# Kernel tuning notes

Hardware: AMD Instinct MI355X
Metric: run time of the kernel (lower is better)

Reference implementation:

```python
import jax, jax.numpy as jnp
import numpy as np

B, V, M, L, D, OUT = 16, 16, 32, 24, 128, 193
VOCAB = {'cond': 5000, 'proc': 2000, 'drug': 600, 'lab_item': 700, 'lab_value': 200, 'inj_item': 400, 'inj_value': 200}


def setup_inputs() -> dict:
    key = jax.random.key(0)
    ks = iter(jax.random.split(key, 48))
    def emb_table(v):
        t = 0.02 * jax.random.normal(next(ks), (v, D), jnp.float32)
        return t.at[0].set(0.0)  # padding_idx = 0
    inp = {}
    inp['tok_cond'] = jax.random.randint(next(ks), (B, V, L), 0, VOCAB['cond'])
    inp['tok_proc'] = jax.random.randint(next(ks), (B, V, L), 0, VOCAB['proc'])
    inp['tok_drug'] = jax.random.randint(next(ks), (B, V, L), 0, VOCAB['drug'])
    inp['tok_lab_item'] = jax.random.randint(next(ks), (B, V, M, L), 0, VOCAB['lab_item'])
    inp['tok_lab_value'] = jax.random.randint(next(ks), (B, V, M, L), 0, VOCAB['lab_value'])
    inp['tok_inj_item'] = jax.random.randint(next(ks), (B, V, M, L), 0, VOCAB['inj_item'])
    inp['tok_inj_value'] = jax.random.randint(next(ks), (B, V, M, L), 0, VOCAB['inj_value'])
    inp['weight'] = jax.random.uniform(next(ks), (B, V, 1), jnp.float32)
    inp['age'] = jax.random.uniform(next(ks), (B, V, 1), jnp.float32)
    for n in ['cond', 'proc', 'drug', 'lab_item', 'lab_value', 'inj_item', 'inj_value']:
        inp['emb_' + n] = emb_table(VOCAB[n])
    def gru_params(nk):
        s = 0.05
        return (s * jax.random.normal(next(ks), (nk, 3 * D, D), jnp.float32),
                s * jax.random.normal(next(ks), (nk, 3 * D, D), jnp.float32),
                jnp.zeros((nk, 3 * D), jnp.float32),
                jnp.zeros((nk, 3 * D), jnp.float32))
    inp['mgru_wih'], inp['mgru_whh'], inp['mgru_bih'], inp['mgru_bhh'] = gru_params(5)
    inp['vgru_wih'], inp['vgru_whh'], inp['vgru_bih'], inp['vgru_bhh'] = gru_params(7)
    inp['info_w'] = 0.05 * jax.random.normal(next(ks), (2, D), jnp.float32)  # Linear(1, D) weights for weight/age
    inp['info_b'] = jnp.zeros((2, D), jnp.float32)
    inp['fc_w'] = 0.05 * jax.random.normal(next(ks), (7 * D, OUT), jnp.float32)
    inp['fc_b'] = jnp.zeros((OUT,), jnp.float32)
    return inp


def _gru(x, wih, whh, bih, bhh):
    # x: [N, T, Din]; torch nn.GRU semantics, gate order (r, z, n), h0 = 0
    n_, t_, _ = x.shape
    d = whh.shape[1]
    xg = jnp.einsum('ntd,gd->ntg', x, wih) + bih  # precompute input gates [N, T, 3D]
    def step(h, xg_t):
        gh = h @ whh.T + bhh
        ir, iz, inn = jnp.split(xg_t, 3, axis=-1)
        hr, hz, hn = jnp.split(gh, 3, axis=-1)
        r = jax.nn.sigmoid(ir + hr)
        z = jax.nn.sigmoid(iz + hz)
        n = jnp.tanh(inn + r * hn)
        h2 = (1.0 - z) * n + z * h
        return h2, h2
    h0 = jnp.zeros((n_, d), x.dtype)
    hT, outs = jax.lax.scan(step, h0, jnp.swapaxes(xg, 0, 1))
    return jnp.swapaxes(outs, 0, 1), hT  # output [N,T,D], hidden [N,D]

_gru_keys = jax.vmap(_gru)  # vmap over the per-feature-key leading axis


def reference(tok_cond, tok_proc, tok_drug, tok_lab_item, tok_lab_value, tok_inj_item, tok_inj_value,
              weight, age, emb_cond, emb_proc, emb_drug, emb_lab_item, emb_lab_value, emb_inj_item,
              emb_inj_value, mgru_wih, mgru_whh, mgru_bih, mgru_bhh, vgru_wih, vgru_whh, vgru_bih,
              vgru_bhh, info_w, info_b, fc_w, fc_b):
    b, v, m, _ = tok_lab_item.shape
    d = emb_cond.shape[1]
    # visit-event features: embedding + sum over code dim (dropout = identity, eval mode)
    e_cond = emb_cond[tok_cond].sum(axis=2)  # [B,V,D]
    e_proc = emb_proc[tok_proc].sum(axis=2)
    e_drug = emb_drug[tok_drug].sum(axis=2)
    # monitor-event pairs: elementwise mul of the two embeddings, sum over code dim
    lab = (emb_lab_item[tok_lab_item] * emb_lab_value[tok_lab_value]).sum(axis=3)  # [B,V,M,D]
    inj = (emb_inj_item[tok_inj_item] * emb_inj_value[tok_inj_value]).sum(axis=3)
    # repeat visit embeddings across the monitor axis (repeat(1, max_monitors, 1))
    rep = lambda e: jnp.broadcast_to(e[:, :, None, :], (b, v, m, d))
    mon_in = jnp.stack([rep(e_cond), rep(e_proc), rep(e_drug), lab, inj], axis=0)
    mon_in = mon_in.reshape(5, b * v, m, d)  # aggregate_tensors with uniform lengths
    # per-key monitor-level GRUs
    mon_out, mon_h = _gru_keys(mon_in, mgru_wih, mgru_whh, mgru_bih, mgru_bhh)
    # split_tensor + extract_and_transpose: take last monitor step per visit -> [5,B,V,D]
    last = mon_out[:, :, -1, :].reshape(5, b, v, d)
    # patient info Linear(1, D) for weight / age
    w_emb = weight * info_w[0] + info_b[0]  # [B,V,D]
    a_emb = age * info_w[1] + info_b[1]
    vis_in = jnp.concatenate([last, jnp.stack([w_emb, a_emb], axis=0)], axis=0)  # [7,B,V,D]
    # per-key visit-level GRUs
    _, vis_h = _gru_keys(vis_in, vgru_wih, vgru_whh, vgru_bih, vgru_bhh)  # [7,B,D]
    patient_emb = jnp.transpose(vis_h, (1, 0, 2)).reshape(b, 7 * d)  # concatenate_patient_embeddings
    logits = jax.nn.relu(patient_emb) @ fc_w + fc_b  # fc_patient: ReLU -> Linear(7D, output_size)
    return logits
```

## Files before the change

### kernel.cpp

```cpp
#include <hip/hip_runtime.h>
#include <stdint.h>

typedef unsigned short u16;
typedef unsigned int u32;

#define B_ 16
#define V_ 16
#define M_ 32
#define L_ 24
#define D_ 128
#define G_ 384
#define N_ 256
#define NM_ 8192
#define OUT_ 193

using bf16x8 = __attribute__((ext_vector_type(8))) __bf16;
using floatx4 = __attribute__((ext_vector_type(4))) float;
using u16x4 = __attribute__((ext_vector_type(4))) u16;

__device__ __forceinline__ float bf2f(u16 u) {
  u32 x = ((u32)u) << 16;
  return __builtin_bit_cast(float, x);
}
__device__ __forceinline__ u16 f2bf(float f) {
  u32 u = __builtin_bit_cast(u32, f);
  u = (u + 0x7FFFu + ((u >> 16) & 1u)) >> 16;
  return (u16)u;
}
__device__ __forceinline__ float sigm_(float x) {
  return __builtin_amdgcn_rcpf(1.0f + __expf(-x));
}
__device__ __forceinline__ float tanh_(float x) {
  float e = __expf(2.0f * x);
  return 1.0f - 2.0f * __builtin_amdgcn_rcpf(e + 1.0f);
}
__device__ __forceinline__ floatx4 mfma16(bf16x8 a, bf16x8 b, floatx4 c) {
  return __builtin_amdgcn_mfma_f32_16x16x32_bf16(a, b, c, 0, 0, 0);
}
__device__ __forceinline__ void stage16(const u16* gsrc, u16* ldst) {
  __builtin_amdgcn_global_load_lds(
      (const __attribute__((address_space(1))) void*)gsrc,
      (__attribute__((address_space(3))) void*)ldst, 16, 0, 0);
}

__device__ __forceinline__ void split4(floatx4 v, u16* __restrict__ hip, u16* __restrict__ lop) {
  u16x4 h, l;
#pragma unroll
  for (int k = 0; k < 4; k++) {
    u16 hb = f2bf(v[k]);
    h[k] = hb;
    l[k] = f2bf(v[k] - bf2f(hb));
  }
  *(u16x4*)hip = h;
  *(u16x4*)lop = l;
}

#define CONVB 1152
#define VEB 32
#define PEB 1024

__global__ __launch_bounds__(256) void k_stage1(
    const int* __restrict__ tc, const int* __restrict__ tp, const int* __restrict__ td,
    const int* __restrict__ tli, const int* __restrict__ tlv,
    const int* __restrict__ tii, const int* __restrict__ tiv,
    const float* __restrict__ ec, const float* __restrict__ ep, const float* __restrict__ ed,
    const float* __restrict__ eli, const float* __restrict__ elv,
    const float* __restrict__ eii, const float* __restrict__ eiv,
    const float* __restrict__ wv, const float* __restrict__ av,
    const float* __restrict__ iw, const float* __restrict__ ib,
    const float* __restrict__ mwih, const float* __restrict__ vwih,
    const float* __restrict__ mwhh, const float* __restrict__ vwhh,
    u16* __restrict__ wih_hi, u16* __restrict__ whh_hi,
    u16* __restrict__ ce_hi, u16* __restrict__ ce_lo,
    u16* __restrict__ vx_hi, u16* __restrict__ vx_lo,
    u16* __restrict__ mx_hi, u16* __restrict__ mx_lo) {
  int blk = blockIdx.x, tid = threadIdx.x;
  if (blk < CONVB) {
    const int SW = 12 * G_ * D_, S5 = 5 * G_ * D_;
    int i4 = (blk * 256 + tid) * 4;
    floatx4 v;
    u16* dst;
    if (i4 < SW) {
      v = *(const floatx4*)(i4 < S5 ? mwih + i4 : vwih + (i4 - S5));
      dst = wih_hi + i4;
    } else {
      int o = i4 - SW;
      v = *(const floatx4*)(o < S5 ? mwhh + o : vwhh + (o - S5));
      dst = whh_hi + o;
    }
    u16x4 h;
#pragma unroll
    for (int k = 0; k < 4; k++) h[k] = f2bf(v[k]);
    *(u16x4*)dst = h;
  } else if (blk < CONVB + VEB) {
    int n = (blk - CONVB) * 8 + (tid >> 5);
    int j = tid & 31;
    floatx4 a0 = {0.f, 0.f, 0.f, 0.f}, a1 = a0, a2 = a0;
#pragma unroll 4
    for (int l = 0; l < L_; l++) {
      a0 += *(const floatx4*)(ec + (size_t)tc[n * L_ + l] * D_ + j * 4);
      a1 += *(const floatx4*)(ep + (size_t)tp[n * L_ + l] * D_ + j * 4);
      a2 += *(const floatx4*)(ed + (size_t)td[n * L_ + l] * D_ + j * 4);
    }
    size_t o0 = (size_t)n * D_ + j * 4;
    split4(a0, ce_hi + o0, ce_lo + o0);
    split4(a1, ce_hi + (size_t)N_ * D_ + o0, ce_lo + (size_t)N_ * D_ + o0);
    split4(a2, ce_hi + (size_t)2 * N_ * D_ + o0, ce_lo + (size_t)2 * N_ * D_ + o0);
    float wq = wv[n], aq = av[n];
    floatx4 iw0 = *(const floatx4*)(iw + j * 4);
    floatx4 iw1 = *(const floatx4*)(iw + D_ + j * 4);
    floatx4 ib0 = *(const floatx4*)(ib + j * 4);
    floatx4 ib1 = *(const floatx4*)(ib + D_ + j * 4);
    floatx4 v1 = wq * iw0 + ib0;
    floatx4 v2 = aq * iw1 + ib1;
    split4(v1, vx_hi + (size_t)5 * N_ * D_ + o0, vx_lo + (size_t)5 * N_ * D_ + o0);
    split4(v2, vx_hi + (size_t)6 * N_ * D_ + o0, vx_lo + (size_t)6 * N_ * D_ + o0);
  } else {
    int r = (blk - CONVB - VEB) * 8 + (tid >> 5);
    int j = tid & 31;
    floatx4 al4 = {0.f, 0.f, 0.f, 0.f}, ai4 = al4;
#pragma unroll 4
    for (int l = 0; l < L_; l++) {
      al4 += *(const floatx4*)(eli + (size_t)tli[r * L_ + l] * D_ + j * 4) *
             *(const floatx4*)(elv + (size_t)tlv[r * L_ + l] * D_ + j * 4);
      ai4 += *(const floatx4*)(eii + (size_t)tii[r * L_ + l] * D_ + j * 4) *
             *(const floatx4*)(eiv + (size_t)tiv[r * L_ + l] * D_ + j * 4);
    }
    size_t o = (size_t)r * D_ + j * 4;
    split4(al4, mx_hi + o, mx_lo + o);
    split4(ai4, mx_hi + (size_t)NM_ * D_ + o, mx_lo + (size_t)NM_ * D_ + o);
  }
}

template <int MODE, int TT>
__global__ __launch_bounds__(512, 1) void k_gru8(
    int cpk,
    const u16* __restrict__ xa_hi, const u16* __restrict__ xa_lo,
    const u16* __restrict__ xb_hi, const u16* __restrict__ xb_lo,
    const u16* __restrict__ wih_all, const float* __restrict__ bih_all,
    const u16* __restrict__ whh_all, const float* __restrict__ bhh_all,
    u16* __restrict__ out_hi, u16* __restrict__ out_lo, float* __restrict__ out_f32) {
  int key = blockIdx.x / cpk;
  int chunk = blockIdx.x - key * cpk;
  int n0 = chunk * 16;
  const u16* whh = whh_all + (size_t)key * (G_ * D_);
  const u16* wih = wih_all + (size_t)key * (G_ * D_);

  __shared__ __align__(16) u16 hls[2][2][16 * 128];
  __shared__ __align__(16) u16 xls[2][2][16 * 128];

  int tid = threadIdx.x;
  int w = tid >> 6, lane = tid & 63, mq = lane & 15, q = lane >> 4;
  int dA = (w << 4) + mq;

  int sp = tid >> 8, sr = (tid >> 4) & 15, sc = tid & 15;
  u16* ldst0 = &xls[0][0][0] + (size_t)sp * (16 * 128) + (sr * 16 + sc) * 8;
  u16* ldst1 = &xls[1][0][0] + (size_t)sp * (16 * 128) + (sr * 16 + sc) * 8;
  const bool constx = (MODE == 0) && (key < 3);
  const u16* gsrc;
  {
    const u16* hi;
    const u16* lo;
    size_t grow;
    if (MODE == 0) {
      if (key < 3) { hi = xa_hi; lo = xa_lo; grow = (size_t)key * N_ + n0 + sr; }
      else         { hi = xb_hi; lo = xb_lo; grow = (size_t)(key - 3) * NM_ + (size_t)(n0 + sr) * M_; }
    } else {
      hi = xa_hi; lo = xa_lo; grow = (size_t)key * N_ + sr * 16;
    }
    gsrc = (sp ? lo : hi) + grow * D_ + ((sc ^ sr) * 8);
  }

  bf16x8 bw[3][4], wf[3][4];
#pragma unroll
  for (int g = 0; g < 3; g++)
#pragma unroll
    for (int kk = 0; kk < 4; kk++) {
      size_t ro = (size_t)(g * 128 + dA) * D_ + kk * 32 + q * 8;
      bw[g][kk] = *(const bf16x8*)(whh + ro);
      wf[g][kk] = *(const bf16x8*)(wih + ro);
    }
  floatx4 bseed[3], bxs[3];
#pragma unroll
  for (int g = 0; g < 3; g++) {
    float bh = bhh_all[key * G_ + g * 128 + dA];
    float bi = bih_all[key * G_ + g * 128 + dA];
    bseed[g] = {bh, bh, bh, bh};
    bxs[g] = {bi, bi, bi, bi};
  }

  stage16(gsrc, ldst0);
  __syncthreads();

  floatx4 accx[3];
  if (constx) {
    const u16* xp0 = &xls[0][0][0];
    const u16* xp1 = &xls[0][1][0];
    bf16x8 xh[4], xl[4];
#pragma unroll
    for (int kk = 0; kk < 4; kk++) {
      int off = mq * 128 + (((kk * 4 + q) ^ mq) * 8);
      xh[kk] = *(const bf16x8*)(xp0 + off);
      xl[kk] = *(const bf16x8*)(xp1 + off);
    }
#pragma unroll
    for (int g = 0; g < 3; g++) {
      floatx4 a = mfma16(xh[0], wf[g][0], bxs[g]);
      a = mfma16(xl[0], wf[g][0], a);
      a = mfma16(xh[1], wf[g][1], a);
      a = mfma16(xl[1], wf[g][1], a);
      a = mfma16(xh[2], wf[g][2], a);
      a = mfma16(xl[2], wf[g][2], a);
      a = mfma16(xh[3], wf[g][3], a);
      accx[g] = mfma16(xl[3], wf[g][3], a);
    }
  }

  float h_old[4];
#pragma unroll
  for (int k = 0; k < 4; k++) h_old[k] = 0.f;

#pragma unroll 2
  for (int t = 0; t < TT; ++t) {
    int slot = t & 1;
    if (!constx && (t + 1 < TT))
      stage16(gsrc + (size_t)(t + 1) * D_, slot ? ldst0 : ldst1);
    if (!constx) {
      const u16* xp0 = &xls[slot][0][0];
      const u16* xp1 = &xls[slot][1][0];
      bf16x8 xh[4], xl[4];
#pragma unroll
      for (int kk = 0; kk < 4; kk++) {
        int off = mq * 128 + (((kk * 4 + q) ^ mq) * 8);
        xh[kk] = *(const bf16x8*)(xp0 + off);
        xl[kk] = *(const bf16x8*)(xp1 + off);
      }
#pragma unroll
      for (int g = 0; g < 3; g++) {
        floatx4 a = mfma16(xh[0], wf[g][0], bxs[g]);
        a = mfma16(xl[0], wf[g][0], a);
        a = mfma16(xh[1], wf[g][1], a);
        a = mfma16(xl[1], wf[g][1], a);
        a = mfma16(xh[2], wf[g][2], a);
        a = mfma16(xl[2], wf[g][2], a);
        a = mfma16(xh[3], wf[g][3], a);
        accx[g] = mfma16(xl[3], wf[g][3], a);
      }
    }
    floatx4 acch[3];
    if (t > 0) {
      const u16* hp0 = &hls[(t - 1) & 1][0][0];
      const u16* hp1 = &hls[(t - 1) & 1][1][0];
      bf16x8 ah[4], al[4];
#pragma unroll
      for (int kk = 0; kk < 4; kk++) {
        int off = mq * 128 + (((kk * 4 + q) ^ mq) * 8);
        ah[kk] = *(const bf16x8*)(hp0 + off);
        al[kk] = *(const bf16x8*)(hp1 + off);
      }
#pragma unroll
      for (int g = 0; g < 3; g++) {
        floatx4 a = mfma16(ah[0], bw[g][0], bseed[g]);
        a = mfma16(al[0], bw[g][0], a);
        a = mfma16(ah[1], bw[g][1], a);
        a = mfma16(al[1], bw[g][1], a);
        a = mfma16(ah[2], bw[g][2], a);
        a = mfma16(al[2], bw[g][2], a);
        a = mfma16(ah[3], bw[g][3], a);
        acch[g] = mfma16(al[3], bw[g][3], a);
      }
    } else {
#pragma unroll
      for (int g = 0; g < 3; g++) acch[g] = bseed[g];
    }
    u16* wrh = &hls[slot][0][0];
    u16* wrl = &hls[slot][1][0];
#pragma unroll
    for (int i = 0; i < 4; i++) {
      int row = q * 4 + i;
      float r = sigm_(accx[0][i] + acch[0][i]);
      float z = sigm_(accx[1][i] + acch[1][i]);
      float nn = tanh_(accx[2][i] + r * acch[2][i]);
      float h2 = (1.0f - z) * nn + z * h_old[i];
      h_old[i] = h2;
      u32 ub = __builtin_bit_cast(u32, h2);
      u16 hb = (u16)(ub >> 16);
      float rem = h2 - __builtin_bit_cast(float, ub & 0xFFFF0000u);
      u16 lb = f2bf(rem);
      if (t == TT - 1) {
        if (MODE == 0) {
          size_t o = ((size_t)key * N_ + n0 + row) * D_ + dA;
          out_hi[o] = hb;
          out_lo[o] = lb;
        } else {
          out_f32[((size_t)key * 16 + row) * D_ + dA] = h2;
        }
      } else {
        int idx = row * 128 + (((dA >> 3) ^ row) * 8) + (dA & 7);
        wrh[idx] = hb;
        wrl[idx] = lb;
      }
    }
    if (t + 1 < TT) __syncthreads();
  }
}

__global__ __launch_bounds__(256) void k_fc(
    const float* __restrict__ vis_h, const float* __restrict__ fc_w,
    const float* __restrict__ fc_b, float* __restrict__ out) {
  int b = blockIdx.x;
  int cg = blockIdx.y;
  int tid = threadIdx.x;
  int j = tid & 15, s = tid >> 4;
  int c = cg * 16 + j;
  bool cv = c < OUT_;

  __shared__ float hbuf[7 * D_];
  __shared__ float red[16][16];
  for (int i = tid; i < 7 * D_; i += 256) {
    float v = vis_h[((size_t)(i >> 7) * 16 + b) * D_ + (i & 127)];
    hbuf[i] = v > 0.f ? v : 0.f;
  }
  __syncthreads();

  float acc = 0.f;
  if (cv) {
    const float* wp = fc_w + (size_t)(s * 56) * OUT_ + c;
#pragma unroll 8
    for (int k = 0; k < 56; k++) acc += hbuf[s * 56 + k] * wp[(size_t)k * OUT_];
  }
  red[s][j] = acc;
  __syncthreads();
  if (s == 0 && cv) {
    float t = 0.f;
#pragma unroll
    for (int m = 0; m < 16; m++) t += red[m][j];
    out[(size_t)b * OUT_ + c] = t + fc_b[c];
  }
}

extern "C" void kernel_launch(void* const* d_in, const int* in_sizes, int n_in,
                              void* d_out, int out_size, void* d_ws, size_t ws_size,
                              hipStream_t stream) {
  (void)in_sizes; (void)n_in; (void)out_size; (void)ws_size;
  const int* tok_cond = (const int*)d_in[0];
  const int* tok_proc = (const int*)d_in[1];
  const int* tok_drug = (const int*)d_in[2];
  const int* tok_lab_item = (const int*)d_in[3];
  const int* tok_lab_value = (const int*)d_in[4];
  const int* tok_inj_item = (const int*)d_in[5];
  const int* tok_inj_value = (const int*)d_in[6];
  const float* weight = (const float*)d_in[7];
  const float* age = (const float*)d_in[8];
  const float* emb_cond = (const float*)d_in[9];
  const float* emb_proc = (const float*)d_in[10];
  const float* emb_drug = (const float*)d_in[11];
  const float* emb_lab_item = (const float*)d_in[12];
  const float* emb_lab_value = (const float*)d_in[13];
  const float* emb_inj_item = (const float*)d_in[14];
  const float* emb_inj_value = (const float*)d_in[15];
  const float* mgru_wih = (const float*)d_in[16];
  const float* mgru_whh = (const float*)d_in[17];
  const float* mgru_bih = (const float*)d_in[18];
  const float* mgru_bhh = (const float*)d_in[19];
  const float* vgru_wih = (const float*)d_in[20];
  const float* vgru_whh = (const float*)d_in[21];
  const float* vgru_bih = (const float*)d_in[22];
  const float* vgru_bhh = (const float*)d_in[23];
  const float* info_w = (const float*)d_in[24];
  const float* info_b = (const float*)d_in[25];
  const float* fc_w = (const float*)d_in[26];
  const float* fc_b = (const float*)d_in[27];

  char* p = (char*)d_ws;
  auto take = [&](size_t bytes) { char* r = p; p += (bytes + 255) & ~(size_t)255; return r; };
  u16* mx_hi = (u16*)take((size_t)2 * NM_ * D_ * 2);
  u16* mx_lo = (u16*)take((size_t)2 * NM_ * D_ * 2);
  u16* ce_hi = (u16*)take((size_t)3 * N_ * D_ * 2);
  u16* ce_lo = (u16*)take((size_t)3 * N_ * D_ * 2);
  u16* vx_hi = (u16*)take((size_t)7 * N_ * D_ * 2);
  u16* vx_lo = (u16*)take((size_t)7 * N_ * D_ * 2);
  float* vis_h = (float*)take((size_t)7 * 16 * D_ * 4);
  u16* wih_hi = (u16*)take((size_t)12 * G_ * D_ * 2);
  u16* whh_hi = (u16*)take((size_t)12 * G_ * D_ * 2);

  k_stage1<<<CONVB + VEB + PEB, 256, 0, stream>>>(
      tok_cond, tok_proc, tok_drug, tok_lab_item, tok_lab_value, tok_inj_item, tok_inj_value,
      emb_cond, emb_proc, emb_drug, emb_lab_item, emb_lab_value, emb_inj_item, emb_inj_value,
      weight, age, info_w, info_b, mgru_wih, vgru_wih, mgru_whh, vgru_whh,
      wih_hi, whh_hi, ce_hi, ce_lo, vx_hi, vx_lo, mx_hi, mx_lo);
  k_gru8<0, 32><<<80, 512, 0, stream>>>(16, ce_hi, ce_lo, mx_hi, mx_lo,
                                        wih_hi, mgru_bih, whh_hi, mgru_bhh,
                                        vx_hi, vx_lo, nullptr);
  k_gru8<1, 16><<<7, 512, 0, stream>>>(1, vx_hi, vx_lo, nullptr, nullptr,
                                       wih_hi + (size_t)5 * G_ * D_, vgru_bih,
                                       whh_hi + (size_t)5 * G_ * D_, vgru_bhh,
                                       nullptr, nullptr, vis_h);
  k_fc<<<dim3(B_, 13), 256, 0, stream>>>(vis_h, fc_w, fc_b, (float*)d_out);
}
```

Before: 224.5 us.

## Fuse monitor and visit GRU kernels with per-key atomic flag dependencies

Merges the monitor-level GRU launch (80 blocks) and the visit-level GRU launch (7 blocks) into one 87-block kernel. Visit blocks for keys 5-6 (weight/age) start at once, and visit blocks for keys 0-4 spin on a per-key atomic counter until all 16 monitor chunks for that key have written their outputs. This removes one kernel launch and the global barrier between the two stages, and lets unrelated keys overlap. The cost is a memset per call and spin-wait blocks that occupy CUs, which relies on all 87 blocks being co-resident to avoid deadlock.

```diff
diff --git a/kernel.cpp b/kernel.cpp
--- a/kernel.cpp
+++ b/kernel.cpp
@@ -133,29 +133,24 @@
 }
 
 template <int MODE, int TT>
-__global__ __launch_bounds__(512, 1) void k_gru8(
-    int cpk,
+__device__ __forceinline__ void gru_body(
+    int key, int n0,
     const u16* __restrict__ xa_hi, const u16* __restrict__ xa_lo,
     const u16* __restrict__ xb_hi, const u16* __restrict__ xb_lo,
     const u16* __restrict__ wih_all, const float* __restrict__ bih_all,
     const u16* __restrict__ whh_all, const float* __restrict__ bhh_all,
-    u16* __restrict__ out_hi, u16* __restrict__ out_lo, float* __restrict__ out_f32) {
-  int key = blockIdx.x / cpk;
-  int chunk = blockIdx.x - key * cpk;
-  int n0 = chunk * 16;
+    u16* __restrict__ out_hi, u16* __restrict__ out_lo, float* __restrict__ out_f32,
+    u16* hls_, u16* xls_) {
   const u16* whh = whh_all + (size_t)key * (G_ * D_);
   const u16* wih = wih_all + (size_t)key * (G_ * D_);
-
-  __shared__ __align__(16) u16 hls[2][2][16 * 128];
-  __shared__ __align__(16) u16 xls[2][2][16 * 128];
 
   int tid = threadIdx.x;
   int w = tid >> 6, lane = tid & 63, mq = lane & 15, q = lane >> 4;
   int dA = (w << 4) + mq;
 
   int sp = tid >> 8, sr = (tid >> 4) & 15, sc = tid & 15;
-  u16* ldst0 = &xls[0][0][0] + (size_t)sp * (16 * 128) + (sr * 16 + sc) * 8;
-  u16* ldst1 = &xls[1][0][0] + (size_t)sp * (16 * 128) + (sr * 16 + sc) * 8;
+  u16* ldst0 = xls_ + (size_t)sp * (16 * 128) + (sr * 16 + sc) * 8;
+  u16* ldst1 = xls_ + (size_t)(2 + sp) * (16 * 128) + (sr * 16 + sc) * 8;
   const bool constx = (MODE == 0) && (key < 3);
   const u16* gsrc;
   {
@@ -194,8 +189,8 @@
 
   floatx4 accx[3];
   if (constx) {
-    const u16* xp0 = &xls[0][0][0];
-    const u16* xp1 = &xls[0][1][0];
+    const u16* xp0 = xls_;
+    const u16* xp1 = xls_ + (16 * 128);
     bf16x8 xh[4], xl[4];
 #pragma unroll
     for (int kk = 0; kk < 4; kk++) {
@@ -226,8 +221,8 @@
     if (!constx && (t + 1 < TT))
       stage16(gsrc + (size_t)(t + 1) * D_, slot ? ldst0 : ldst1);
     if (!constx) {
-      const u16* xp0 = &xls[slot][0][0];
-      const u16* xp1 = &xls[slot][1][0];
+      const u16* xp0 = xls_ + (size_t)(slot * 2) * (16 * 128);
+      const u16* xp1 = xls_ + (size_t)(slot * 2 + 1) * (16 * 128);
       bf16x8 xh[4], xl[4];
 #pragma unroll
       for (int kk = 0; kk < 4; kk++) {
@@ -249,8 +244,8 @@
     }
     floatx4 acch[3];
     if (t > 0) {
-      const u16* hp0 = &hls[(t - 1) & 1][0][0];
-      const u16* hp1 = &hls[(t - 1) & 1][1][0];
+      const u16* hp0 = hls_ + (size_t)(((t - 1) & 1) * 2) * (16 * 128);
+      const u16* hp1 = hls_ + (size_t)(((t - 1) & 1) * 2 + 1) * (16 * 128);
       bf16x8 ah[4], al[4];
 #pragma unroll
       for (int kk = 0; kk < 4; kk++) {
@@ -273,8 +268,8 @@
 #pragma unroll
       for (int g = 0; g < 3; g++) acch[g] = bseed[g];
     }
-    u16* wrh = &hls[slot][0][0];
-    u16* wrl = &hls[slot][1][0];
+    u16* wrh = hls_ + (size_t)(slot * 2) * (16 * 128);
+    u16* wrl = hls_ + (size_t)(slot * 2 + 1) * (16 * 128);
 #pragma unroll
     for (int i = 0; i < 4; i++) {
       int row = q * 4 + i;
@@ -302,6 +297,44 @@
       }
     }
     if (t + 1 < TT) __syncthreads();
+  }
+}
+
+__global__ __launch_bounds__(512, 1) void k_mega(
+    const u16* __restrict__ ce_hi, const u16* __restrict__ ce_lo,
+    const u16* __restrict__ mx_hi, const u16* __restrict__ mx_lo,
+    u16* vx_hi, u16* vx_lo,
+    const u16* __restrict__ wih_m, const float* __restrict__ bih_m,
+    const u16* __restrict__ whh_m, const float* __restrict__ bhh_m,
+    const u16* __restrict__ wih_v, const float* __restrict__ bih_v,
+    const u16* __restrict__ whh_v, const float* __restrict__ bhh_v,
+    float* __restrict__ vis_h, u32* flags) {
+  __shared__ __align__(16) u16 hls[2][2][16 * 128];
+  __shared__ __align__(16) u16 xls[2][2][16 * 128];
+  int blk = blockIdx.x;
+  if (blk < 80) {
+    int key = blk >> 4, chunk = blk & 15;
+    gru_body<0, 32>(key, chunk * 16, ce_hi, ce_lo, mx_hi, mx_lo,
+                    wih_m, bih_m, whh_m, bhh_m,
+                    vx_hi, vx_lo, nullptr, &hls[0][0][0], &xls[0][0][0]);
+    __syncthreads();
+    if (threadIdx.x == 0) {
+      __threadfence();
+      __hip_atomic_fetch_add(&flags[key], 1u, __ATOMIC_RELEASE, __HIP_MEMORY_SCOPE_AGENT);
+    }
+  } else {
+    int key = blk - 80;
+    if (key < 5) {
+      if (threadIdx.x == 0) {
+        while (__hip_atomic_load(&flags[key], __ATOMIC_ACQUIRE, __HIP_MEMORY_SCOPE_AGENT) < 16u)
+          __builtin_amdgcn_s_sleep(8);
+      }
+      __syncthreads();
+      __threadfence();
+    }
+    gru_body<1, 16>(key, 0, vx_hi, vx_lo, nullptr, nullptr,
+                    wih_v, bih_v, whh_v, bhh_v,
+                    nullptr, nullptr, vis_h, &hls[0][0][0], &xls[0][0][0]);
   }
 }
 
@@ -383,18 +416,19 @@
   float* vis_h = (float*)take((size_t)7 * 16 * D_ * 4);
   u16* wih_hi = (u16*)take((size_t)12 * G_ * D_ * 2);
   u16* whh_hi = (u16*)take((size_t)12 * G_ * D_ * 2);
+  u32* flags = (u32*)take(256);
+
+  hipMemsetAsync(flags, 0, 64, stream);
 
   k_stage1<<<CONVB + VEB + PEB, 256, 0, stream>>>(
       tok_cond, tok_proc, tok_drug, tok_lab_item, tok_lab_value, tok_inj_item, tok_inj_value,
       emb_cond, emb_proc, emb_drug, emb_lab_item, emb_lab_value, emb_inj_item, emb_inj_value,
       weight, age, info_w, info_b, mgru_wih, vgru_wih, mgru_whh, vgru_whh,
       wih_hi, whh_hi, ce_hi, ce_lo, vx_hi, vx_lo, mx_hi, mx_lo);
-  k_gru8<0, 32><<<80, 512, 0, stream>>>(16, ce_hi, ce_lo, mx_hi, mx_lo,
-                                        wih_hi, mgru_bih, whh_hi, mgru_bhh,
-                                        vx_hi, vx_lo, nullptr);
-  k_gru8<1, 16><<<7, 512, 0, stream>>>(1, vx_hi, vx_lo, nullptr, nullptr,
-                                       wih_hi + (size_t)5 * G_ * D_, vgru_bih,
-                                       whh_hi + (size_t)5 * G_ * D_, vgru_bhh,
-                                       nullptr, nullptr, vis_h);
+  k_mega<<<87, 512, 0, stream>>>(
+      ce_hi, ce_lo, mx_hi, mx_lo, vx_hi, vx_lo,
+      wih_hi, mgru_bih, whh_hi, mgru_bhh,
+      wih_hi + (size_t)5 * G_ * D_, vgru_bih, whh_hi + (size_t)5 * G_ * D_, vgru_bhh,
+      vis_h, flags);
   k_fc<<<dim3(B_, 13), 256, 0, stream>>>(vis_h, fc_w, fc_b, (float*)d_out);
 }
```

Result: slower. 230.2 us (+2.5%).

## Load GRU inputs directly from global into registers, drop LDS staging

Applied to the files above, without the earlier changes.

The GRU kernel previously staged each timestep's x tile into shared memory with global_load_lds, double-buffered. It now has each lane load its own x fragments straight from global memory into registers, prefetching the next timestep after the input MFMAs. The per-step __syncthreads is replaced by a custom barrier that waits only on LDS/scalar counters, not on vector memory loads. This is meant to remove the LDS round trip and let global prefetches overlap the barrier. In exchange, each wave issues its own redundant global loads, and the register prefetch holds extra VGPRs.

```diff
diff --git a/kernel.cpp b/kernel.cpp
--- a/kernel.cpp
+++ b/kernel.cpp
@@ -37,10 +37,8 @@
 __device__ __forceinline__ floatx4 mfma16(bf16x8 a, bf16x8 b, floatx4 c) {
   return __builtin_amdgcn_mfma_f32_16x16x32_bf16(a, b, c, 0, 0, 0);
 }
-__device__ __forceinline__ void stage16(const u16* gsrc, u16* ldst) {
-  __builtin_amdgcn_global_load_lds(
-      (const __attribute__((address_space(1))) void*)gsrc,
-      (__attribute__((address_space(3))) void*)ldst, 16, 0, 0);
+__device__ __forceinline__ void lds_barrier() {
+  asm volatile("s_waitcnt lgkmcnt(0)\n\ts_barrier" ::: "memory");
 }
 
 __device__ __forceinline__ void split4(floatx4 v, u16* __restrict__ hip, u16* __restrict__ lop) {
@@ -147,28 +145,19 @@
   const u16* wih = wih_all + (size_t)key * (G_ * D_);
 
   __shared__ __align__(16) u16 hls[2][2][16 * 128];
-  __shared__ __align__(16) u16 xls[2][2][16 * 128];
 
   int tid = threadIdx.x;
   int w = tid >> 6, lane = tid & 63, mq = lane & 15, q = lane >> 4;
   int dA = (w << 4) + mq;
 
-  int sp = tid >> 8, sr = (tid >> 4) & 15, sc = tid & 15;
-  u16* ldst0 = &xls[0][0][0] + (size_t)sp * (16 * 128) + (sr * 16 + sc) * 8;
-  u16* ldst1 = &xls[1][0][0] + (size_t)sp * (16 * 128) + (sr * 16 + sc) * 8;
   const bool constx = (MODE == 0) && (key < 3);
-  const u16* gsrc;
-  {
-    const u16* hi;
-    const u16* lo;
-    size_t grow;
-    if (MODE == 0) {
-      if (key < 3) { hi = xa_hi; lo = xa_lo; grow = (size_t)key * N_ + n0 + sr; }
-      else         { hi = xb_hi; lo = xb_lo; grow = (size_t)(key - 3) * NM_ + (size_t)(n0 + sr) * M_; }
-    } else {
-      hi = xa_hi; lo = xa_lo; grow = (size_t)key * N_ + sr * 16;
-    }
-    gsrc = (sp ? lo : hi) + grow * D_ + ((sc ^ sr) * 8);
+  const u16 *xhb, *xlb;
+  size_t xbase, TS;
+  if (MODE == 0) {
+    if (key < 3) { xhb = xa_hi; xlb = xa_lo; xbase = ((size_t)key * N_ + n0 + mq) * D_; TS = 0; }
+    else { xhb = xb_hi; xlb = xb_lo; xbase = ((size_t)(key - 3) * NM_ + (size_t)(n0 + mq) * M_) * D_; TS = D_; }
+  } else {
+    xhb = xa_hi; xlb = xa_lo; xbase = ((size_t)key * N_ + mq * 16) * D_; TS = D_;
   }
 
   bf16x8 bw[3][4], wf[3][4];
@@ -189,20 +178,15 @@
     bxs[g] = {bi, bi, bi, bi};
   }
 
-  stage16(gsrc, ldst0);
-  __syncthreads();
+  bf16x8 xh[4], xl[4];
+#pragma unroll
+  for (int kk = 0; kk < 4; kk++) {
+    xh[kk] = *(const bf16x8*)(xhb + xbase + kk * 32 + q * 8);
+    xl[kk] = *(const bf16x8*)(xlb + xbase + kk * 32 + q * 8);
+  }
 
   floatx4 accx[3];
   if (constx) {
-    const u16* xp0 = &xls[0][0][0];
-    const u16* xp1 = &xls[0][1][0];
-    bf16x8 xh[4], xl[4];
-#pragma unroll
-    for (int kk = 0; kk < 4; kk++) {
-      int off = mq * 128 + (((kk * 4 + q) ^ mq) * 8);
-      xh[kk] = *(const bf16x8*)(xp0 + off);
-      xl[kk] = *(const bf16x8*)(xp1 + off);
-    }
 #pragma unroll
     for (int g = 0; g < 3; g++) {
       floatx4 a = mfma16(xh[0], wf[g][0], bxs[g]);
@@ -222,19 +206,7 @@
 
 #pragma unroll 2
   for (int t = 0; t < TT; ++t) {
-    int slot = t & 1;
-    if (!constx && (t + 1 < TT))
-      stage16(gsrc + (size_t)(t + 1) * D_, slot ? ldst0 : ldst1);
     if (!constx) {
-      const u16* xp0 = &xls[slot][0][0];
-      const u16* xp1 = &xls[slot][1][0];
-      bf16x8 xh[4], xl[4];
-#pragma unroll
-      for (int kk = 0; kk < 4; kk++) {
-        int off = mq * 128 + (((kk * 4 + q) ^ mq) * 8);
-        xh[kk] = *(const bf16x8*)(xp0 + off);
-        xl[kk] = *(const bf16x8*)(xp1 + off);
-      }
 #pragma unroll
       for (int g = 0; g < 3; g++) {
         floatx4 a = mfma16(xh[0], wf[g][0], bxs[g]);
@@ -246,6 +218,14 @@
         a = mfma16(xh[3], wf[g][3], a);
         accx[g] = mfma16(xl[3], wf[g][3], a);
       }
+      if (t + 1 < TT) {
+        size_t xo = xbase + (size_t)(t + 1) * TS;
+#pragma unroll
+        for (int kk = 0; kk < 4; kk++) {
+          xh[kk] = *(const bf16x8*)(xhb + xo + kk * 32 + q * 8);
+          xl[kk] = *(const bf16x8*)(xlb + xo + kk * 32 + q * 8);
+        }
+      }
     }
     floatx4 acch[3];
     if (t > 0) {
@@ -273,8 +253,8 @@
 #pragma unroll
       for (int g = 0; g < 3; g++) acch[g] = bseed[g];
     }
-    u16* wrh = &hls[slot][0][0];
-    u16* wrl = &hls[slot][1][0];
+    u16* wrh = &hls[t & 1][0][0];
+    u16* wrl = &hls[t & 1][1][0];
 #pragma unroll
     for (int i = 0; i < 4; i++) {
       int row = q * 4 + i;
@@ -301,7 +281,7 @@
         wrl[idx] = lb;
       }
     }
-    if (t + 1 < TT) __syncthreads();
+    if (t + 1 < TT) lds_barrier();
   }
 }
 
```

New measurement: 265.8 us. 18.4% more time.
